# Kernel tuning notes

Measured on AMD Instinct MI355X. Metric: run time of the kernel, lower is better.

Reference implementation:

```python
import jax, jax.numpy as jnp
import numpy as np

D_MODEL = 3072
N_HEADS = 24
MAX_LEN = 2048
ROPE_THETA = 10000.0
DH = D_MODEL // N_HEADS                  # 128
Q_PROJ = D_MODEL // 2                    # 1536
KV_PROJ = 2 * D_MODEL // 3               # 2048
NOPE = DH // 2                           # 64
ROPE = DH // 2                           # 64
EPS = 1e-5


def layernorm(x, w, b):
    m = jnp.mean(x, axis=-1, keepdims=True)
    v = jnp.mean(jnp.square(x - m), axis=-1, keepdims=True)
    return (x - m) / jnp.sqrt(v + EPS) * w + b


def rotate_half(x):
    h = x.shape[-1] // 2
    return jnp.concatenate([-x[..., h:], x[..., :h]], axis=-1)


def rope_tables(S):
    freqs = 1.0 / ROPE_THETA ** (jnp.arange(0, DH, 2, dtype=jnp.float32) / DH)  # [DH/2]
    emb = jnp.arange(S, dtype=jnp.float32)[:, None] * freqs[None, :]            # [S, DH/2]
    # torch: take first ROPE//2 freqs then .repeat(...,2) => tile along last axis
    cos = jnp.tile(jnp.cos(emb)[:, : ROPE // 2], (1, 2))  # [S, ROPE]
    sin = jnp.tile(jnp.sin(emb)[:, : ROPE // 2], (1, 2))
    return cos[None, None], sin[None, None]               # [1,1,S,ROPE]


def setup_inputs() -> dict:
    key = jax.random.key(0)
    ks = jax.random.split(key, 7)
    x = jax.random.normal(ks[0], (2, 2048, D_MODEL), dtype=jnp.float32)
    p = lambda k, shp: 0.01 * jax.random.normal(k, shp, dtype=jnp.float32)
    return {
        "x": x,
        "W_dq": p(ks[1], (D_MODEL, Q_PROJ)),
        "W_uq": p(ks[2], (Q_PROJ, D_MODEL)),
        "q_ln_w": jnp.ones((Q_PROJ,), jnp.float32),
        "q_ln_b": jnp.zeros((Q_PROJ,), jnp.float32),
        "W_dkv": p(ks[3], (D_MODEL, KV_PROJ + ROPE)),
        "W_ukv": p(ks[4], (KV_PROJ, D_MODEL + N_HEADS * NOPE)),
        "kv_ln_w": jnp.ones((KV_PROJ,), jnp.float32),
        "kv_ln_b": jnp.zeros((KV_PROJ,), jnp.float32),
        "W_o": p(ks[5], (D_MODEL, D_MODEL)),
    }


def reference(x, W_dq, W_uq, q_ln_w, q_ln_b, W_dkv, W_ukv, kv_ln_w, kv_ln_b, W_o):
    B, S, D = x.shape
    cos, sin = rope_tables(S)  # past_length=0, S_full=S

    # Q path: low-rank down/up projection
    cq = layernorm(x @ W_dq, q_ln_w, q_ln_b)          # [B,S,Q_PROJ]
    Q = (cq @ W_uq).reshape(B, S, N_HEADS, DH).transpose(0, 2, 1, 3)  # [B,H,S,DH]
    Q_nope, Q_rope = Q[..., :NOPE], Q[..., NOPE:]
    Q_rope = Q_rope * cos + rotate_half(Q_rope) * sin

    # KV path
    compressed_kv = x @ W_dkv                          # [B,S,KV_PROJ+ROPE]
    KV_lora = layernorm(compressed_kv[..., :KV_PROJ], kv_ln_w, kv_ln_b)
    K_rope = compressed_kv[..., KV_PROJ:]              # [B,S,ROPE]
    KV = (KV_lora @ W_ukv).reshape(B, S, N_HEADS, DH + NOPE).transpose(0, 2, 1, 3)
    K_nope, V = KV[..., :NOPE], KV[..., NOPE:]         # [B,H,S,NOPE], [B,H,S,DH]

    K_rope = K_rope[:, None]                           # [B,1,S,ROPE] shared head
    K_rope = K_rope * cos + rotate_half(K_rope) * sin

    q = jnp.concatenate([Q_nope, Q_rope], axis=-1)     # [B,H,S,DH]
    # k = cat(K_nope, K_rope broadcast over heads)
    k = jnp.concatenate([K_nope, jnp.broadcast_to(K_rope, (B, N_HEADS, S, ROPE))], axis=-1)

    scale = 1.0 / jnp.sqrt(jnp.float32(DH))
    scores = jnp.einsum("bhqd,bhkd->bhqk", q, k) * scale
    causal = jnp.tril(jnp.ones((S, S), dtype=bool))
    scores = jnp.where(causal[None, None], scores, jnp.float32(-jnp.inf))
    attn = jax.nn.softmax(scores, axis=-1)
    out = jnp.einsum("bhqk,bhkd->bhqd", attn, V)
    out = out.transpose(0, 2, 1, 3).reshape(B, S, D)
    out = out @ W_o.T
    return out, compressed_kv
```

## Files before the change

### kernel.cpp

```cpp
#include <hip/hip_runtime.h>

typedef unsigned short u16;
typedef __attribute__((ext_vector_type(8))) short short8;
typedef __attribute__((ext_vector_type(4))) float f32x4;

#define NROWS   4096
#define S_LEN   2048
#define NHEADS  24
#define DMODEL  3072
#define QPROJ   1536
#define KVPROJ  2048
#define CKV_W   2112
#define UKV_N   4608

__device__ __forceinline__ float bf2f(u16 v) {
    unsigned u = ((unsigned)v) << 16; float f; __builtin_memcpy(&f, &u, 4); return f;
}
__device__ __forceinline__ u16 f2bf(float f) {
    unsigned u; __builtin_memcpy(&u, &f, 4);
    u = (u + 0x7FFFu + ((u >> 16) & 1u)) >> 16; return (u16)u;
}
__device__ __forceinline__ void async16(const u16* g, u16* l) {
    __builtin_amdgcn_global_load_lds((const __attribute__((address_space(1))) unsigned int*)g,
                                     (__attribute__((address_space(3))) unsigned int*)l,
                                     16, 0, 0);
}

__global__ void conv_bf16(const float* __restrict__ X, u16* __restrict__ Y, int n) {
    int i = (blockIdx.x * 256 + threadIdx.x) * 4;
    if (i >= n) return;
    float4 v = *(const float4*)(X + i);
    Y[i+0] = f2bf(v.x); Y[i+1] = f2bf(v.y); Y[i+2] = f2bf(v.z); Y[i+3] = f2bf(v.w);
}

__global__ void transpose_bf16(const float* __restrict__ W, u16* __restrict__ WT,
                               int K, int N, float scale) {
    __shared__ float t[32][33];
    int nb = blockIdx.x * 32, kb = blockIdx.y * 32;
    int c = threadIdx.x & 31, rq = threadIdx.x >> 5;
#pragma unroll
    for (int i = 0; i < 4; ++i) {
        int r = rq * 4 + i;
        t[r][c] = W[(size_t)(kb + r) * N + nb + c];
    }
    __syncthreads();
#pragma unroll
    for (int i = 0; i < 4; ++i) {
        int r = rq * 4 + i;
        WT[(size_t)(nb + r) * K + kb + c] = f2bf(t[c][r] * scale);
    }
}

__global__ __launch_bounds__(256) void ln_kernel(const float* __restrict__ X, int ldx,
                                                 const float* __restrict__ g,
                                                 const float* __restrict__ b,
                                                 u16* __restrict__ Y, int W) {
    int row = blockIdx.x;
    const float* x = X + (size_t)row * ldx;
    float s = 0.f, s2 = 0.f;
    for (int i = threadIdx.x; i < W; i += 256) { float v = x[i]; s += v; s2 += v * v; }
#pragma unroll
    for (int off = 32; off >= 1; off >>= 1) { s += __shfl_xor(s, off); s2 += __shfl_xor(s2, off); }
    __shared__ float red[8];
    int w = threadIdx.x >> 6;
    if ((threadIdx.x & 63) == 0) { red[w] = s; red[4 + w] = s2; }
    __syncthreads();
    s  = red[0] + red[1] + red[2] + red[3];
    s2 = red[4] + red[5] + red[6] + red[7];
    float mean = s / W;
    float var  = s2 / W - mean * mean;
    float rstd = rsqrtf(var + 1e-5f);
    u16* y = Y + (size_t)row * W;
    for (int i = threadIdx.x; i < W; i += 256)
        y[i] = f2bf((x[i] - mean) * rstd * g[i] + b[i]);
}

__global__ void rope_q_kernel(u16* __restrict__ Q) {
    int idx = blockIdx.x * 256 + threadIdx.x;
    int j = idx & 31; int t = idx >> 5; int h = t % NHEADS; int row = t / NHEADS;
    int s = row & (S_LEN - 1);
    float freq = __expf(-(float)j * (9.210340371976184f / 64.f));
    float ang = (float)s * freq;
    float c = cosf(ang), si = sinf(ang);
    u16* p = Q + (size_t)row * DMODEL + h * 128 + 64;
    float x1 = bf2f(p[j]), x2 = bf2f(p[j + 32]);
    p[j]      = f2bf(x1 * c - x2 * si);
    p[j + 32] = f2bf(x2 * c + x1 * si);
}

__global__ void rope_k_kernel(const float* __restrict__ ckv, u16* __restrict__ kr) {
    int idx = blockIdx.x * 256 + threadIdx.x;
    int j = idx & 31; int row = idx >> 5;
    int s = row & (S_LEN - 1);
    float freq = __expf(-(float)j * (9.210340371976184f / 64.f));
    float ang = (float)s * freq;
    float c = cosf(ang), si = sinf(ang);
    const float* src = ckv + (size_t)row * CKV_W + KVPROJ;
    float x1 = src[j], x2 = src[j + 32];
    kr[(size_t)row * 64 + j]      = f2bf(x1 * c - x2 * si);
    kr[(size_t)row * 64 + j + 32] = f2bf(x2 * c + x1 * si);
}

__global__ __launch_bounds__(256) void pack_k(const u16* __restrict__ KVb,
                                              const u16* __restrict__ kr,
                                              u16* __restrict__ Kp) {
    int bh = blockIdx.y, bb = bh / NHEADS, h = bh % NHEADS;
    int s0 = blockIdx.x * 64;
    int t = threadIdx.x;
    size_t base = (size_t)bb * S_LEN;
#pragma unroll
    for (int it = 0; it < 4; ++it) {
        int j = it * 256 + t;
        int r = j >> 4, cb = (j & 15) * 8;
        int s = s0 + r;
        uint4 v;
        if (cb < 64) v = *(const uint4*)&KVb[(base + s) * UKV_N + h * 192 + cb];
        else         v = *(const uint4*)&kr[(base + s) * 64 + (cb - 64)];
        *(uint4*)&Kp[((size_t)bh * S_LEN + s) * 128 + cb] = v;
    }
}

__global__ __launch_bounds__(256) void pack_v(const u16* __restrict__ KVb,
                                              u16* __restrict__ Vt) {
    __shared__ u16 tile[64][136];
    int bh = blockIdx.y, bb = bh / NHEADS, h = bh % NHEADS;
    int s0 = blockIdx.x * 64;
    int t = threadIdx.x;
    size_t base = (size_t)bb * S_LEN;
#pragma unroll
    for (int it = 0; it < 4; ++it) {
        int j = it * 256 + t;
        int r = j >> 4, cb = (j & 15) * 8;
        *(uint4*)&tile[r][cb] = *(const uint4*)&KVb[(base + s0 + r) * UKV_N + h * 192 + 64 + cb];
    }
    __syncthreads();
#pragma unroll
    for (int it = 0; it < 4; ++it) {
        int j = it * 256 + t;
        int d = j >> 3, sb = (j & 7) * 8;
        u16 tmp[8];
#pragma unroll
        for (int e = 0; e < 8; ++e) tmp[e] = tile[sb + e][d];
        *(uint4*)&Vt[((size_t)bh * 128 + d) * S_LEN + s0 + sb] = *(uint4*)tmp;
    }
}

template<bool OUT_BF16>
__global__ __launch_bounds__(256) void gemm_nt(const u16* __restrict__ A,
                                               const u16* __restrict__ B,
                                               void* __restrict__ Cv,
                                               int M, int N, int K, int nx) {
    __shared__ u16 a_lds[2][128][32];
    __shared__ u16 b_lds[2][128][32];
    int nwg = (int)gridDim.x;
    int bid = (int)blockIdx.x;
    int wg = (bid & 7) * (nwg >> 3) + (bid >> 3);
    int by = wg / nx, bx = wg - by * nx;
    int m0 = by * 128, n0 = bx * 128;
    int tid = threadIdx.x, lane = tid & 63, w = tid >> 6;
    int wm = w >> 1, wn = w & 1;
    int srow = lane >> 2;
    int kx = (lane >> 4) & 2;
    int scol = ((lane & 3) ^ kx) * 8;
    int r0 = w * 32 + srow, r1 = w * 32 + 16 + srow;
    const u16* A0 = A + (size_t)(m0 + r0) * K + scol;
    const u16* A1 = A + (size_t)(m0 + r1) * K + scol;
    int bn0 = n0 + r0; if (bn0 >= N) bn0 = N - 1;
    int bn1 = n0 + r1; if (bn1 >= N) bn1 = N - 1;
    const u16* B0 = B + (size_t)bn0 * K + scol;
    const u16* B1 = B + (size_t)bn1 * K + scol;
    char* aB = (char*)&a_lds[0][0][0];
    char* bB = (char*)&b_lds[0][0][0];
    int d0 = w * 2048, d1 = w * 2048 + 1024;
    int cb = ((lane >> 4) * 16) ^ ((lane & 8) << 2);

    f32x4 acc[4][4] = {};
    async16(A0, (u16*)(aB + d0)); async16(A1, (u16*)(aB + d1));
    async16(B0, (u16*)(bB + d0)); async16(B1, (u16*)(bB + d1));
    __syncthreads();
    int buf = 0;
    for (int kb = 0; kb < K; kb += 32) {
        if (kb + 32 < K) {
            int ob = (buf ^ 1) * 8192;
            async16(A0 + kb + 32, (u16*)(aB + ob + d0));
            async16(A1 + kb + 32, (u16*)(aB + ob + d1));
            async16(B0 + kb + 32, (u16*)(bB + ob + d0));
            async16(B1 + kb + 32, (u16*)(bB + ob + d1));
        }
        const char* ab = aB + buf * 8192;
        const char* bb = bB + buf * 8192;
        short8 af[4], bf[4];
#pragma unroll
        for (int i = 0; i < 4; ++i) {
            af[i] = *(const short8*)(ab + (wm * 64 + i * 16 + (lane & 15)) * 64 + cb);
            bf[i] = *(const short8*)(bb + (wn * 64 + i * 16 + (lane & 15)) * 64 + cb);
        }
#pragma unroll
        for (int i = 0; i < 4; ++i)
#pragma unroll
            for (int j = 0; j < 4; ++j)
                acc[i][j] = __builtin_amdgcn_mfma_f32_16x16x32_bf16(af[i], bf[j], acc[i][j], 0, 0, 0);
        __syncthreads();
        buf ^= 1;
    }
#pragma unroll
    for (int i = 0; i < 4; ++i) {
        int row = m0 + wm * 64 + i * 16 + ((lane >> 4) << 2);
#pragma unroll
        for (int j = 0; j < 4; ++j) {
            int col = n0 + wn * 64 + j * 16 + (lane & 15);
            if (col < N) {
#pragma unroll
                for (int r = 0; r < 4; ++r) {
                    if (OUT_BF16) ((u16*)Cv)[(size_t)(row + r) * N + col] = f2bf(acc[i][j][r]);
                    else          ((float*)Cv)[(size_t)(row + r) * N + col] = acc[i][j][r];
                }
            }
        }
    }
}

__global__ __launch_bounds__(256) void attn_kernel(const u16* __restrict__ Qb,
                                                   const u16* __restrict__ Kp,
                                                   const u16* __restrict__ Vt,
                                                   u16* __restrict__ AO) {
    __shared__ u16 k_lds[64][128];
    __shared__ u16 v_lds[128][64];
    __shared__ u16 p_lds[4][16][72];
    int bid = blockIdx.x;
    int jj = bid >> 3;
    int bh = (bid & 7) * 6 + (jj >> 4);
    int bx = jj & 15;
    int bb = bh / NHEADS, h = bh % NHEADS;
    int tid = threadIdx.x, lane = tid & 63, w = tid >> 6;
    size_t base = (size_t)bb * S_LEN;
    size_t bhS = (size_t)bh * S_LEN;

    const char* Kbyte = (const char*)Kp;
    const char* Vbyte = (const char*)Vt;
    char* kB = (char*)&k_lds[0][0];
    char* vB = (char*)&v_lds[0][0];
    size_t ksrc[4], vsrc[4];
    int kd[4];
#pragma unroll
    for (int is = 0; is < 4; ++is) {
        int j = is * 256 + tid;
        int r = j >> 4;
        int cbs = ((j & 15) * 16) ^ ((r & 7) << 4);
        ksrc[is] = (bhS + r) * 256 + cbs;
        int d = j >> 3;
        int kbs = (((j & 7) ^ (d & 7)) * 16);
        vsrc[is] = ((size_t)bh * 128 + d) * (S_LEN * 2) + kbs;
        kd[is] = (is * 256 + w * 64) * 16;
    }

    for (int seg = 0; seg < 2; ++seg) {
        int qx = seg == 0 ? (31 - bx) : bx;
        int q0 = qx * 64;

        short8 qf[4];
        {
            int qrow = q0 + w * 16 + (lane & 15);
            const u16* qp = Qb + (base + qrow) * DMODEL + h * 128 + ((lane >> 4) * 8);
#pragma unroll
            for (int ks = 0; ks < 4; ++ks) qf[ks] = *(const short8*)(qp + ks * 32);
        }

        f32x4 acc_o[8] = {};
        float m_run[4], l_run[4];
#pragma unroll
        for (int r = 0; r < 4; ++r) { m_run[r] = -1e30f; l_run[r] = 0.f; }

        int ntiles = qx + 1;
        for (int t = 0; t < ntiles; ++t) {
            size_t kv0 = (size_t)t * 64;
#pragma unroll
            for (int is = 0; is < 4; ++is)
                async16((const u16*)(Kbyte + ksrc[is] + kv0 * 256), (u16*)(kB + kd[is]));
#pragma unroll
            for (int is = 0; is < 4; ++is)
                async16((const u16*)(Vbyte + vsrc[is] + kv0 * 2), (u16*)(vB + kd[is]));
            __syncthreads();

            f32x4 sc[4];
            __builtin_amdgcn_s_setprio(1);
#pragma unroll
            for (int nb = 0; nb < 4; ++nb) {
                f32x4 a = {};
                int row = nb * 16 + (lane & 15);
                const char* kb_ = kB + row * 256;
                int x = (row & 7) << 4;
#pragma unroll
                for (int ks = 0; ks < 4; ++ks) {
                    short8 kf = *(const short8*)(kb_ + ((ks * 64 + (lane >> 4) * 16) ^ x));
                    a = __builtin_amdgcn_mfma_f32_16x16x32_bf16(qf[ks], kf, a, 0, 0, 0);
                }
                sc[nb] = a;
            }
            __builtin_amdgcn_s_setprio(0);

            if (t == qx) {
                int kvb = t * 64;
                int qg = q0 + w * 16 + ((lane >> 4) << 2);
#pragma unroll
                for (int nb = 0; nb < 4; ++nb) {
                    int kc = kvb + nb * 16 + (lane & 15);
#pragma unroll
                    for (int r = 0; r < 4; ++r)
                        if (kc > qg + r) sc[nb][r] = -1e30f;
                }
            }
            float rmax[4];
#pragma unroll
            for (int r = 0; r < 4; ++r)
                rmax[r] = fmaxf(fmaxf(sc[0][r], sc[1][r]), fmaxf(sc[2][r], sc[3][r]));
#pragma unroll
            for (int off = 1; off < 16; off <<= 1)
#pragma unroll
                for (int r = 0; r < 4; ++r) rmax[r] = fmaxf(rmax[r], __shfl_xor(rmax[r], off));

            bool ok = (rmax[0] <= m_run[0]) & (rmax[1] <= m_run[1]) &
                      (rmax[2] <= m_run[2]) & (rmax[3] <= m_run[3]);
            if (!__all(ok)) {
                float fac[4];
#pragma unroll
                for (int r = 0; r < 4; ++r) {
                    float mnew = fmaxf(m_run[r], rmax[r]);
                    fac[r] = __expf(m_run[r] - mnew);
                    m_run[r] = mnew;
                    l_run[r] *= fac[r];
                }
#pragma unroll
                for (int db = 0; db < 8; ++db)
#pragma unroll
                    for (int r = 0; r < 4; ++r) acc_o[db][r] *= fac[r];
            }
#pragma unroll
            for (int nb = 0; nb < 4; ++nb)
#pragma unroll
                for (int r = 0; r < 4; ++r) {
                    float p = __expf(sc[nb][r] - m_run[r]);
                    sc[nb][r] = p; l_run[r] += p;
                }

#pragma unroll
            for (int nb = 0; nb < 4; ++nb)
#pragma unroll
                for (int r = 0; r < 4; ++r)
                    p_lds[w][((lane >> 4) << 2) + r][nb * 16 + (lane & 15)] = f2bf(sc[nb][r]);
            __builtin_amdgcn_sched_barrier(0);
            __builtin_amdgcn_s_setprio(1);
#pragma unroll
            for (int ks = 0; ks < 2; ++ks) {
                short8 pf = *(const short8*)&p_lds[w][lane & 15][ks * 32 + (lane >> 4) * 8];
#pragma unroll
                for (int db = 0; db < 8; ++db) {
                    int row = db * 16 + (lane & 15);
                    const char* vb_ = vB + row * 128;
                    short8 vf = *(const short8*)(vb_ + ((ks * 64 + (lane >> 4) * 16) ^ ((row & 7) << 4)));
                    acc_o[db] = __builtin_amdgcn_mfma_f32_16x16x32_bf16(pf, vf, acc_o[db], 0, 0, 0);
                }
            }
            __builtin_amdgcn_s_setprio(0);
            __syncthreads();
        }

#pragma unroll
        for (int off = 1; off < 16; off <<= 1)
#pragma unroll
            for (int r = 0; r < 4; ++r) l_run[r] += __shfl_xor(l_run[r], off);

        int orow = q0 + w * 16 + ((lane >> 4) << 2);
#pragma unroll
        for (int db = 0; db < 8; ++db)
#pragma unroll
            for (int r = 0; r < 4; ++r) {
                float o = acc_o[db][r] / l_run[r];
                AO[(base + orow + r) * DMODEL + h * 128 + db * 16 + (lane & 15)] = f2bf(o);
            }
    }
}

extern "C" void kernel_launch(void* const* d_in, const int* in_sizes, int n_in,
                              void* d_out, int out_size, void* d_ws, size_t ws_size,
                              hipStream_t stream) {
    (void)in_sizes; (void)n_in; (void)out_size; (void)ws_size;
    const float* x      = (const float*)d_in[0];
    const float* W_dq   = (const float*)d_in[1];
    const float* W_uq   = (const float*)d_in[2];
    const float* q_ln_w = (const float*)d_in[3];
    const float* q_ln_b = (const float*)d_in[4];
    const float* W_dkv  = (const float*)d_in[5];
    const float* W_ukv  = (const float*)d_in[6];
    const float* kv_ln_w= (const float*)d_in[7];
    const float* kv_ln_b= (const float*)d_in[8];
    const float* W_o    = (const float*)d_in[9];

    float* out = (float*)d_out;
    float* ckv = out + (size_t)NROWS * DMODEL;

    char* ws = (char*)d_ws;
    const size_t OFF_WDQT  = 0;
    const size_t OFF_WUQT  = 9437184;
    const size_t OFF_WDKVT = 18874368;
    const size_t OFF_WUKVT = 31850496;
    const size_t OFF_WO    = 50724864;
    const size_t OFF_XB    = 69599232;
    const size_t OFF_QB    = 94765056;
    const size_t OFF_KVB   = 119930880;
    const size_t OFF_KR    = 157679616;
    const size_t OFF_SLABA = 158203904;
    const size_t OFF_SLABB = 183369728;
    const size_t OFF_KP    = 0;
    const size_t OFF_VT    = OFF_XB;

    u16* Wdq_t  = (u16*)(ws + OFF_WDQT);
    u16* Wuq_t  = (u16*)(ws + OFF_WUQT);
    u16* Wdkv_t = (u16*)(ws + OFF_WDKVT);
    u16* Wukv_t = (u16*)(ws + OFF_WUKVT);
    u16* Wo_b   = (u16*)(ws + OFF_WO);
    u16* xb     = (u16*)(ws + OFF_XB);
    u16* qb     = (u16*)(ws + OFF_QB);
    u16* KVb    = (u16*)(ws + OFF_KVB);
    u16* kr     = (u16*)(ws + OFF_KR);
    float* t0   = (float*)(ws + OFF_SLABA);
    u16* ao     = (u16*)(ws + OFF_SLABA);
    u16* cq     = (u16*)(ws + OFF_SLABB);
    u16* kvl    = (u16*)(ws + OFF_SLABB);
    u16* Kp     = (u16*)(ws + OFF_KP);
    u16* Vt     = (u16*)(ws + OFF_VT);

    const float SCALE = 0.08838834764831845f;

    transpose_bf16<<<dim3(QPROJ / 32, DMODEL / 32), 256, 0, stream>>>(W_dq,  Wdq_t,  DMODEL, QPROJ, 1.0f);
    transpose_bf16<<<dim3(DMODEL / 32, QPROJ / 32), 256, 0, stream>>>(W_uq,  Wuq_t,  QPROJ, DMODEL, SCALE);
    transpose_bf16<<<dim3(CKV_W / 32, DMODEL / 32), 256, 0, stream>>>(W_dkv, Wdkv_t, DMODEL, CKV_W, 1.0f);
    transpose_bf16<<<dim3(UKV_N / 32, KVPROJ / 32), 256, 0, stream>>>(W_ukv, Wukv_t, KVPROJ, UKV_N, 1.0f);
    conv_bf16<<<9216, 256, 0, stream>>>(W_o, Wo_b, DMODEL * DMODEL);
    conv_bf16<<<12288, 256, 0, stream>>>(x, xb, NROWS * DMODEL);

    gemm_nt<false><<<(QPROJ / 128) * (NROWS / 128), 256, 0, stream>>>(xb, Wdq_t, t0, NROWS, QPROJ, DMODEL, QPROJ / 128);
    ln_kernel<<<NROWS, 256, 0, stream>>>(t0, QPROJ, q_ln_w, q_ln_b, cq, QPROJ);
    gemm_nt<true><<<(DMODEL / 128) * (NROWS / 128), 256, 0, stream>>>(cq, Wuq_t, qb, NROWS, DMODEL, QPROJ, DMODEL / 128);
    rope_q_kernel<<<12288, 256, 0, stream>>>(qb);

    gemm_nt<false><<<17 * (NROWS / 128), 256, 0, stream>>>(xb, Wdkv_t, ckv, NROWS, CKV_W, DMODEL, 17);
    ln_kernel<<<NROWS, 256, 0, stream>>>(ckv, CKV_W, kv_ln_w, kv_ln_b, kvl, KVPROJ);
    rope_k_kernel<<<512, 256, 0, stream>>>(ckv, kr);
    gemm_nt<true><<<(UKV_N / 128) * (NROWS / 128), 256, 0, stream>>>(kvl, Wukv_t, KVb, NROWS, UKV_N, KVPROJ, UKV_N / 128);

    pack_k<<<dim3(S_LEN / 64, 2 * NHEADS), 256, 0, stream>>>(KVb, kr, Kp);
    pack_v<<<dim3(S_LEN / 64, 2 * NHEADS), 256, 0, stream>>>(KVb, Vt);

    attn_kernel<<<768, 256, 0, stream>>>(qb, Kp, Vt, ao);

    gemm_nt<false><<<(DMODEL / 128) * (NROWS / 128), 256, 0, stream>>>(ao, Wo_b, out, NROWS, DMODEL, DMODEL, DMODEL / 128);
}
```

Baseline: 646.1 us.

## Triple-buffer GEMM LDS tiles with partial vmcnt waits for deeper prefetch

The bf16 NT GEMM's double-buffered LDS pipeline becomes a three-stage ring buffer that prefetches two K-tiles ahead. The full __syncthreads at each step is replaced by an explicit s_waitcnt vmcnt(4) plus s_barrier, so the newest tile's loads can stay in flight across the barrier. This aims to hide more global-load latency behind the MFMA work. In exchange, LDS use rises from 32KB to 48KB per block, which may lower occupancy, and correctness depends on the hand-written waitcnt counts.

```diff
diff --git a/kernel.cpp b/kernel.cpp
--- a/kernel.cpp
+++ b/kernel.cpp
@@ -150,8 +150,8 @@
                                                const u16* __restrict__ B,
                                                void* __restrict__ Cv,
                                                int M, int N, int K, int nx) {
-    __shared__ u16 a_lds[2][128][32];
-    __shared__ u16 b_lds[2][128][32];
+    __shared__ u16 a_lds[3][128][32];
+    __shared__ u16 b_lds[3][128][32];
     int nwg = (int)gridDim.x;
     int bid = (int)blockIdx.x;
     int wg = (bid & 7) * (nwg >> 3) + (bid >> 3);
@@ -173,22 +173,29 @@
     char* bB = (char*)&b_lds[0][0][0];
     int d0 = w * 2048, d1 = w * 2048 + 1024;
     int cb = ((lane >> 4) * 16) ^ ((lane & 8) << 2);
+    int nt = K >> 5;
 
     f32x4 acc[4][4] = {};
-    async16(A0, (u16*)(aB + d0)); async16(A1, (u16*)(aB + d1));
-    async16(B0, (u16*)(bB + d0)); async16(B1, (u16*)(bB + d1));
-    __syncthreads();
-    int buf = 0;
-    for (int kb = 0; kb < K; kb += 32) {
-        if (kb + 32 < K) {
-            int ob = (buf ^ 1) * 8192;
-            async16(A0 + kb + 32, (u16*)(aB + ob + d0));
-            async16(A1 + kb + 32, (u16*)(aB + ob + d1));
-            async16(B0 + kb + 32, (u16*)(bB + ob + d0));
-            async16(B1 + kb + 32, (u16*)(bB + ob + d1));
+    async16(A0, (u16*)(aB + d0));          async16(A1, (u16*)(aB + d1));
+    async16(B0, (u16*)(bB + d0));          async16(B1, (u16*)(bB + d1));
+    async16(A0 + 32, (u16*)(aB + 8192 + d0)); async16(A1 + 32, (u16*)(aB + 8192 + d1));
+    async16(B0 + 32, (u16*)(bB + 8192 + d0)); async16(B1 + 32, (u16*)(bB + 8192 + d1));
+    __builtin_amdgcn_sched_barrier(0);
+    asm volatile("s_waitcnt vmcnt(4)" ::: "memory");
+    asm volatile("s_barrier" ::: "memory");
+    __builtin_amdgcn_sched_barrier(0);
+
+    int o0 = 0, o1 = 8192, o2 = 16384;
+    for (int t = 0; t < nt; ++t) {
+        if (t + 2 < nt) {
+            int kb = (t + 2) * 32;
+            async16(A0 + kb, (u16*)(aB + o2 + d0));
+            async16(A1 + kb, (u16*)(aB + o2 + d1));
+            async16(B0 + kb, (u16*)(bB + o2 + d0));
+            async16(B1 + kb, (u16*)(bB + o2 + d1));
         }
-        const char* ab = aB + buf * 8192;
-        const char* bb = bB + buf * 8192;
+        const char* ab = aB + o0;
+        const char* bb = bB + o0;
         short8 af[4], bf[4];
 #pragma unroll
         for (int i = 0; i < 4; ++i) {
@@ -200,8 +207,12 @@
 #pragma unroll
             for (int j = 0; j < 4; ++j)
                 acc[i][j] = __builtin_amdgcn_mfma_f32_16x16x32_bf16(af[i], bf[j], acc[i][j], 0, 0, 0);
-        __syncthreads();
-        buf ^= 1;
+        __builtin_amdgcn_sched_barrier(0);
+        if (t + 2 < nt) asm volatile("s_waitcnt vmcnt(4)" ::: "memory");
+        else            asm volatile("s_waitcnt vmcnt(0)" ::: "memory");
+        asm volatile("s_barrier" ::: "memory");
+        __builtin_amdgcn_sched_barrier(0);
+        int tmp = o0; o0 = o1; o1 = o2; o2 = tmp;
     }
 #pragma unroll
     for (int i = 0; i < 4; ++i) {
```

New measurement: 662.6 us. +2.5%, slower.
